# Optimization experiments

Hardware: AMD Instinct MI355X
Metric: run time of the kernel (lower is better)

The kernel has to match this reference:

```python
import jax, jax.numpy as jnp
import numpy as np
import math

V, T, E, N = 32000, 128, 64, 1024
SIGMA_MIN, SIGMA_MAX, C = 0.1, 10.0, 2.0


def setup_inputs() -> dict:
    key = jax.random.key(0)
    k1, k2, k3, k4, k5 = jax.random.split(key, 5)
    return {
        "x": jax.random.normal(k1, (T, N), dtype=jnp.float32),
        "mu": jax.random.normal(k2, (V, E), dtype=jnp.float32),
        "log_sigma": jax.random.normal(k3, (V, E), dtype=jnp.float32),
        "mu_c": jax.random.normal(k4, (T, E), dtype=jnp.float32),
        "log_sigma_c": jax.random.normal(k5, (T, E), dtype=jnp.float32),
        "t": 0,
    }


def reference(x, mu, log_sigma, mu_c, log_sigma_c, t):
    # parameter clamping done in-place in the torch forward
    bound = math.sqrt(C)
    mu = jnp.clip(mu, -bound, bound)
    mu_c = jnp.clip(mu_c, -bound, bound)
    log_sigma = jnp.clip(log_sigma, math.log(SIGMA_MIN), math.log(SIGMA_MAX))
    log_sigma_c = jnp.clip(log_sigma_c, math.log(SIGMA_MIN), math.log(SIGMA_MAX))

    sigma = jnp.exp(log_sigma)        # [V, E]
    sigma_c = jnp.exp(log_sigma_c)    # [T, E]

    # pairwise Gaussian expected-likelihood energy, vectorized over topics
    s = sigma[:, None, :] + sigma_c[None, :, :]            # [V, T, E]
    det_fac = jnp.sum(jnp.log(s), axis=-1)                 # [V, T]
    diff = mu[:, None, :] - mu_c[None, :, :]               # [V, T, E]
    diff_mu = jnp.sum(diff * diff / s, axis=-1)            # [V, T]
    emb_dim = mu.shape[-1]
    log_el = -0.5 * (det_fac + diff_mu + emb_dim * math.log(2.0 * math.pi))

    # per-topic softmax over the vocab axis
    w = jax.nn.softmax(log_el, axis=0)                     # [V, T]

    return w @ x.reshape(-1, x.shape[-1])                  # [V, N]
```

## Files before the change

### kernel.cpp

```cpp
#include <hip/hip_runtime.h>
#include <math.h>

#define VV 32000
#define TT 128
#define EE 64
#define NN 1024
#define NPART 500

static constexpr float BOUND    = 1.41421356237309515f;
static constexpr float LOG_SMIN = -2.30258509299404568f;
static constexpr float LOG_SMAX =  2.30258509299404568f;
static constexpr float LN2      =  0.69314718055994531f;
static constexpr float E_LOG2PI =  64.0f * 1.83787706640934548f;

typedef __attribute__((ext_vector_type(2)))  float f32x2;
typedef __attribute__((ext_vector_type(8)))  short short8;
typedef __attribute__((ext_vector_type(16))) float float16;

static __device__ inline unsigned short f2bf(float f) {
    union { float f; unsigned u; } v; v.f = f;
    unsigned r = v.u + 0x7FFFu + ((v.u >> 16) & 1u);
    return (unsigned short)(r >> 16);
}

__global__ __launch_bounds__(256) void prep_ctx(const float* __restrict__ mu_c,
                                                const float* __restrict__ log_sigma_c,
                                                float* __restrict__ sc,
                                                float* __restrict__ mc) {
    int i = blockIdx.x * 256 + threadIdx.x;
    if (i < TT * EE) {
        float ls = log_sigma_c[i];
        ls = fminf(fmaxf(ls, LOG_SMIN), LOG_SMAX);
        sc[i] = __expf(ls);
        float m = mu_c[i];
        mc[i] = fminf(fmaxf(m, -BOUND), BOUND);
    }
}

__global__ __launch_bounds__(256) void logits_kernel(const float* __restrict__ mu,
                                                     const float* __restrict__ log_sigma,
                                                     const float* __restrict__ sc,
                                                     const float* __restrict__ mc,
                                                     float* __restrict__ logitsT,
                                                     float* __restrict__ pm,
                                                     float* __restrict__ pl) {
    __shared__ float part[8][4][64];
    const int tid  = threadIdx.x;
    const int lane = tid & 63;
    const int wv   = tid >> 6;
    const int v0   = blockIdx.x * 64;
    const int t0   = blockIdx.y * 64;
    const int e0   = wv * 16;
    const int e0u  = __builtin_amdgcn_readfirstlane(wv) * 16;

    f32x2 sv[8], mv[8];
    {
        const float* __restrict__ lsp = log_sigma + (size_t)(v0 + lane) * EE + e0;
        const float* __restrict__ mup = mu        + (size_t)(v0 + lane) * EE + e0;
#pragma unroll
        for (int j = 0; j < 8; j++) {
            float a = lsp[2 * j], b = lsp[2 * j + 1];
            a = fminf(fmaxf(a, LOG_SMIN), LOG_SMAX);
            b = fminf(fmaxf(b, LOG_SMIN), LOG_SMAX);
            sv[j] = f32x2{__expf(a), __expf(b)};
            float c = mup[2 * j], d = mup[2 * j + 1];
            mv[j] = f32x2{fminf(fmaxf(c, -BOUND), BOUND), fminf(fmaxf(d, -BOUND), BOUND)};
        }
    }

    for (int tb = 0; tb < 8; tb++) {
        f32x2 q[8], p[8];
#pragma unroll
        for (int i = 0; i < 8; i++) { q[i] = f32x2{0.f, 0.f}; p[i] = f32x2{1.f, 1.f}; }
#pragma unroll
        for (int i = 0; i < 8; i++) {
            const int t = t0 + tb * 8 + i;
            const f32x2* __restrict__ srow = (const f32x2*)(sc + t * EE + e0u);
            const f32x2* __restrict__ mrow = (const f32x2*)(mc + t * EE + e0u);
#pragma unroll
            for (int j = 0; j < 8; j++) {
                f32x2 s = sv[j] + srow[j];
                p[i] *= s;
                f32x2 d = mv[j] - mrow[j];
                f32x2 r;
                r.x = __builtin_amdgcn_rcpf(s.x);
                r.y = __builtin_amdgcn_rcpf(s.y);
                q[i] += d * d * r;
            }
        }
#pragma unroll
        for (int i = 0; i < 8; i++) {
            float contrib = __log2f(p[i].x * p[i].y) * LN2 + q[i].x + q[i].y;
            part[i][wv][lane] = contrib;
        }
        __syncthreads();
#pragma unroll
        for (int k = 0; k < 2; k++) {
            const int i = wv * 2 + k;
            const int t = t0 + tb * 8 + i;
            float sum = part[i][0][lane] + part[i][1][lane] + part[i][2][lane] + part[i][3][lane];
            float logit = -0.5f * (sum + E_LOG2PI);
            logitsT[t * VV + v0 + lane] = logit;

            float m = logit;
#pragma unroll
            for (int off = 1; off < 64; off <<= 1) m = fmaxf(m, __shfl_xor(m, off));
            float sx = __expf(logit - m);
#pragma unroll
            for (int off = 1; off < 64; off <<= 1) sx += __shfl_xor(sx, off);
            if (lane == 0) {
                pm[t * NPART + blockIdx.x] = m;
                pl[t * NPART + blockIdx.x] = sx;
            }
        }
        __syncthreads();
    }
}

__global__ __launch_bounds__(256) void merge_xpose(const float* __restrict__ pm,
                                                   const float* __restrict__ pl,
                                                   const float* __restrict__ x,
                                                   float* __restrict__ stats,
                                                   unsigned short* __restrict__ xT) {
    const int tid = threadIdx.x;
    __shared__ float red[8];
    if (blockIdx.x < TT) {
        const int t = blockIdx.x;
        float m = -3.4e38f;
        for (int j = tid; j < NPART; j += 256) m = fmaxf(m, pm[t * NPART + j]);
#pragma unroll
        for (int off = 1; off < 64; off <<= 1) m = fmaxf(m, __shfl_xor(m, off));
        if ((tid & 63) == 0) red[tid >> 6] = m;
        __syncthreads();
        m = fmaxf(fmaxf(red[0], red[1]), fmaxf(red[2], red[3]));

        float l = 0.0f;
        for (int j = tid; j < NPART; j += 256)
            l += pl[t * NPART + j] * __expf(pm[t * NPART + j] - m);
#pragma unroll
        for (int off = 1; off < 64; off <<= 1) l += __shfl_xor(l, off);
        if ((tid & 63) == 0) red[4 + (tid >> 6)] = l;
        __syncthreads();
        if (tid == 0) {
            float tot = red[4] + red[5] + red[6] + red[7];
            stats[t] = m;
            stats[TT + t] = 1.0f / tot;
        }
    } else {
        const int b = blockIdx.x - TT;
        const int n = b * 128 + (tid & 127);
        const int th = tid >> 7;
        const float* __restrict__ xp = x + n;
#pragma unroll
        for (int i = 0; i < 64; i += 2) {
            int t = th * 64 + i;
            float x0 = xp[(size_t)t * NN];
            float x1 = xp[(size_t)(t + 1) * NN];
            *(unsigned*)&xT[n * TT + t] = (unsigned)f2bf(x0) | ((unsigned)f2bf(x1) << 16);
        }
    }
}

__global__ __launch_bounds__(256) void make_w(const float* __restrict__ logitsT,
                                              const float* __restrict__ stats,
                                              unsigned short* __restrict__ w) {
    __shared__ __attribute__((aligned(16))) unsigned short wl[64][136];
    __shared__ float sl[256];
    const int tid = threadIdx.x;
    const int v0 = blockIdx.x * 64;

    sl[tid] = stats[tid];
    __syncthreads();

    {
        const int v = tid & 63;
        const int tg = tid >> 6;
        const float* __restrict__ lp = logitsT + v0 + v;
#pragma unroll
        for (int i = 0; i < 32; i += 2) {
            int t = tg * 32 + i;
            float lg0 = lp[(size_t)t * VV];
            float lg1 = lp[(size_t)(t + 1) * VV];
            float w0 = __expf(lg0 - sl[t])     * sl[TT + t];
            float w1 = __expf(lg1 - sl[t + 1]) * sl[TT + t + 1];
            *(unsigned*)&wl[v][t] = (unsigned)f2bf(w0) | ((unsigned)f2bf(w1) << 16);
        }
    }
    __syncthreads();

    {
        const int v = tid >> 2;
        const int seg = (tid & 3) * 32;
#pragma unroll
        for (int j = 0; j < 4; j++) {
            uint4 d = *(const uint4*)&wl[v][seg + j * 8];
            *(uint4*)&w[(size_t)(v0 + v) * TT + seg + j * 8] = d;
        }
    }
}

__global__ __launch_bounds__(256) void wx_mfma(const unsigned short* __restrict__ w,
                                               const unsigned short* __restrict__ xT,
                                               float* __restrict__ out) {
    const int tid = threadIdx.x;
    const int v0 = blockIdx.x * 64;
    const int n0 = blockIdx.y * 128;
    const int lane = tid & 63;
    const int wv   = tid >> 6;
    const int vh   = (wv & 1) * 32;
    const int nh   = (wv >> 1) * 64;
    const int r32  = lane & 31;
    const int koff = (lane >> 5) * 8;

    const unsigned short* __restrict__ ap  = w  + (size_t)(v0 + vh + r32) * TT + koff;
    const unsigned short* __restrict__ bp0 = xT + (size_t)(n0 + nh + r32) * TT + koff;
    const unsigned short* __restrict__ bp1 = bp0 + 32 * TT;

    float16 acc0 = {0,0,0,0,0,0,0,0,0,0,0,0,0,0,0,0};
    float16 acc1 = {0,0,0,0,0,0,0,0,0,0,0,0,0,0,0,0};
#pragma unroll
    for (int kb = 0; kb < 8; kb++) {
        short8 a  = *(const short8*)(ap  + kb * 16);
        short8 b0 = *(const short8*)(bp0 + kb * 16);
        short8 b1 = *(const short8*)(bp1 + kb * 16);
        acc0 = __builtin_amdgcn_mfma_f32_32x32x16_bf16(a, b0, acc0, 0, 0, 0);
        acc1 = __builtin_amdgcn_mfma_f32_32x32x16_bf16(a, b1, acc1, 0, 0, 0);
    }

    const int col = lane & 31;
    const int rbase = 4 * (lane >> 5);
#pragma unroll
    for (int r = 0; r < 16; r++) {
        int row = (r & 3) + 8 * (r >> 2) + rbase;
        float* dst = out + (size_t)(v0 + vh + row) * NN + n0 + nh + col;
        dst[0]  = acc0[r];
        dst[32] = acc1[r];
    }
}

extern "C" void kernel_launch(void* const* d_in, const int* in_sizes, int n_in,
                              void* d_out, int out_size, void* d_ws, size_t ws_size,
                              hipStream_t stream) {
    const float* x           = (const float*)d_in[0];
    const float* mu          = (const float*)d_in[1];
    const float* log_sigma   = (const float*)d_in[2];
    const float* mu_c        = (const float*)d_in[3];
    const float* log_sigma_c = (const float*)d_in[4];
    float* out = (float*)d_out;

    float* ws      = (float*)d_ws;
    float* logitsT = ws;
    float* pm      = logitsT + (size_t)TT * VV;
    float* pl      = pm + (size_t)TT * NPART;
    float* stats   = pl + (size_t)TT * NPART;
    float* sc      = stats + 2 * TT;
    float* mc      = sc + TT * EE;
    unsigned short* w_bf16 = (unsigned short*)(mc + TT * EE);
    unsigned short* xT     = w_bf16 + (size_t)VV * TT;

    prep_ctx<<<(TT * EE + 255) / 256, 256, 0, stream>>>(mu_c, log_sigma_c, sc, mc);
    logits_kernel<<<dim3(VV / 64, 2), 256, 0, stream>>>(mu, log_sigma, sc, mc,
                                                        logitsT, pm, pl);
    merge_xpose<<<TT + NN / 128, 256, 0, stream>>>(pm, pl, x, stats, xT);
    make_w<<<VV / 64, 256, 0, stream>>>(logitsT, stats, w_bf16);
    wx_mfma<<<dim3(VV / 64, NN / 128), 256, 0, stream>>>(w_bf16, xT, out);
}
```

Measured before the change: 250.9 us.

## Split logits grid over more topic blocks, prefetch context rows, swap GEMM grid order

Moves the x transpose into the prep kernel, so merge_stats only reduces the softmax statistics. The logits kernel now uses 4 topic blocks of 32 instead of 2 of 64, which doubles the grid. It also loads the context sigma and mu rows into registers ahead of use with a double-buffered prefetch, replacing per-topic global loads. The wx GEMM grid is reordered so consecutive blocks share a w tile across n blocks. The cost is recomputing the clamp and exp of the vocab parameters for twice as many blocks, plus more synchronisation rounds per block.

```diff
diff --git a/kernel.cpp b/kernel.cpp
--- a/kernel.cpp
+++ b/kernel.cpp
@@ -23,17 +23,34 @@
     return (unsigned short)(r >> 16);
 }
 
-__global__ __launch_bounds__(256) void prep_ctx(const float* __restrict__ mu_c,
-                                                const float* __restrict__ log_sigma_c,
-                                                float* __restrict__ sc,
-                                                float* __restrict__ mc) {
-    int i = blockIdx.x * 256 + threadIdx.x;
-    if (i < TT * EE) {
-        float ls = log_sigma_c[i];
-        ls = fminf(fmaxf(ls, LOG_SMIN), LOG_SMAX);
-        sc[i] = __expf(ls);
-        float m = mu_c[i];
-        mc[i] = fminf(fmaxf(m, -BOUND), BOUND);
+__global__ __launch_bounds__(256) void prep_xpose(const float* __restrict__ mu_c,
+                                                  const float* __restrict__ log_sigma_c,
+                                                  const float* __restrict__ x,
+                                                  float* __restrict__ sc,
+                                                  float* __restrict__ mc,
+                                                  unsigned short* __restrict__ xT) {
+    const int tid = threadIdx.x;
+    if (blockIdx.x < 32) {
+        int i = blockIdx.x * 256 + tid;
+        if (i < TT * EE) {
+            float ls = log_sigma_c[i];
+            ls = fminf(fmaxf(ls, LOG_SMIN), LOG_SMAX);
+            sc[i] = __expf(ls);
+            float m = mu_c[i];
+            mc[i] = fminf(fmaxf(m, -BOUND), BOUND);
+        }
+    } else {
+        const int b = blockIdx.x - 32;
+        const int n = b * 128 + (tid & 127);
+        const int th = tid >> 7;
+        const float* __restrict__ xp = x + n;
+#pragma unroll
+        for (int i = 0; i < 64; i += 2) {
+            int t = th * 64 + i;
+            float x0 = xp[(size_t)t * NN];
+            float x1 = xp[(size_t)(t + 1) * NN];
+            *(unsigned*)&xT[n * TT + t] = (unsigned)f2bf(x0) | ((unsigned)f2bf(x1) << 16);
+        }
     }
 }
 
@@ -44,19 +61,18 @@
                                                      float* __restrict__ logitsT,
                                                      float* __restrict__ pm,
                                                      float* __restrict__ pl) {
-    __shared__ float part[8][4][64];
+    __shared__ float part[16][4][64];
     const int tid  = threadIdx.x;
     const int lane = tid & 63;
     const int wv   = tid >> 6;
     const int v0   = blockIdx.x * 64;
-    const int t0   = blockIdx.y * 64;
-    const int e0   = wv * 16;
+    const int t0   = blockIdx.y * 32;
     const int e0u  = __builtin_amdgcn_readfirstlane(wv) * 16;
 
     f32x2 sv[8], mv[8];
     {
-        const float* __restrict__ lsp = log_sigma + (size_t)(v0 + lane) * EE + e0;
-        const float* __restrict__ mup = mu        + (size_t)(v0 + lane) * EE + e0;
+        const float* __restrict__ lsp = log_sigma + (size_t)(v0 + lane) * EE + e0u;
+        const float* __restrict__ mup = mu        + (size_t)(v0 + lane) * EE + e0u;
 #pragma unroll
         for (int j = 0; j < 8; j++) {
             float a = lsp[2 * j], b = lsp[2 * j + 1];
@@ -68,36 +84,45 @@
         }
     }
 
-    for (int tb = 0; tb < 8; tb++) {
-        f32x2 q[8], p[8];
-#pragma unroll
-        for (int i = 0; i < 8; i++) { q[i] = f32x2{0.f, 0.f}; p[i] = f32x2{1.f, 1.f}; }
-#pragma unroll
-        for (int i = 0; i < 8; i++) {
-            const int t = t0 + tb * 8 + i;
-            const f32x2* __restrict__ srow = (const f32x2*)(sc + t * EE + e0u);
-            const f32x2* __restrict__ mrow = (const f32x2*)(mc + t * EE + e0u);
+    f32x2 cs[2][8], cm[2][8];
+    {
+        const f32x2* __restrict__ sp = (const f32x2*)(sc + t0 * EE + e0u);
+        const f32x2* __restrict__ mp = (const f32x2*)(mc + t0 * EE + e0u);
+#pragma unroll
+        for (int j = 0; j < 8; j++) { cs[0][j] = sp[j]; cm[0][j] = mp[j]; }
+    }
+
+    for (int tb = 0; tb < 2; tb++) {
+#pragma unroll
+        for (int i = 0; i < 16; i++) {
+            const int ti  = tb * 16 + i;
+            const int cur = ti & 1;
+            if (ti < 31) {
+                const int tn = t0 + ti + 1;
+                const f32x2* __restrict__ sp = (const f32x2*)(sc + tn * EE + e0u);
+                const f32x2* __restrict__ mp = (const f32x2*)(mc + tn * EE + e0u);
+#pragma unroll
+                for (int j = 0; j < 8; j++) { cs[cur ^ 1][j] = sp[j]; cm[cur ^ 1][j] = mp[j]; }
+            }
+            f32x2 q = {0.f, 0.f};
+            f32x2 p = {1.f, 1.f};
 #pragma unroll
             for (int j = 0; j < 8; j++) {
-                f32x2 s = sv[j] + srow[j];
-                p[i] *= s;
-                f32x2 d = mv[j] - mrow[j];
+                f32x2 s = sv[j] + cs[cur][j];
+                p *= s;
+                f32x2 d = mv[j] - cm[cur][j];
                 f32x2 r;
                 r.x = __builtin_amdgcn_rcpf(s.x);
                 r.y = __builtin_amdgcn_rcpf(s.y);
-                q[i] += d * d * r;
+                q += d * d * r;
             }
-        }
-#pragma unroll
-        for (int i = 0; i < 8; i++) {
-            float contrib = __log2f(p[i].x * p[i].y) * LN2 + q[i].x + q[i].y;
-            part[i][wv][lane] = contrib;
+            part[i][wv][lane] = __log2f(p.x * p.y) * LN2 + q.x + q.y;
         }
         __syncthreads();
 #pragma unroll
-        for (int k = 0; k < 2; k++) {
-            const int i = wv * 2 + k;
-            const int t = t0 + tb * 8 + i;
+        for (int k = 0; k < 4; k++) {
+            const int i = wv * 4 + k;
+            const int t = t0 + tb * 16 + i;
             float sum = part[i][0][lane] + part[i][1][lane] + part[i][2][lane] + part[i][3][lane];
             float logit = -0.5f * (sum + E_LOG2PI);
             logitsT[t * VV + v0 + lane] = logit;
@@ -117,47 +142,31 @@
     }
 }
 
-__global__ __launch_bounds__(256) void merge_xpose(const float* __restrict__ pm,
+__global__ __launch_bounds__(256) void merge_stats(const float* __restrict__ pm,
                                                    const float* __restrict__ pl,
-                                                   const float* __restrict__ x,
-                                                   float* __restrict__ stats,
-                                                   unsigned short* __restrict__ xT) {
-    const int tid = threadIdx.x;
+                                                   float* __restrict__ stats) {
+    const int tid = threadIdx.x;
+    const int t = blockIdx.x;
     __shared__ float red[8];
-    if (blockIdx.x < TT) {
-        const int t = blockIdx.x;
-        float m = -3.4e38f;
-        for (int j = tid; j < NPART; j += 256) m = fmaxf(m, pm[t * NPART + j]);
-#pragma unroll
-        for (int off = 1; off < 64; off <<= 1) m = fmaxf(m, __shfl_xor(m, off));
-        if ((tid & 63) == 0) red[tid >> 6] = m;
-        __syncthreads();
-        m = fmaxf(fmaxf(red[0], red[1]), fmaxf(red[2], red[3]));
-
-        float l = 0.0f;
-        for (int j = tid; j < NPART; j += 256)
-            l += pl[t * NPART + j] * __expf(pm[t * NPART + j] - m);
-#pragma unroll
-        for (int off = 1; off < 64; off <<= 1) l += __shfl_xor(l, off);
-        if ((tid & 63) == 0) red[4 + (tid >> 6)] = l;
-        __syncthreads();
-        if (tid == 0) {
-            float tot = red[4] + red[5] + red[6] + red[7];
-            stats[t] = m;
-            stats[TT + t] = 1.0f / tot;
-        }
-    } else {
-        const int b = blockIdx.x - TT;
-        const int n = b * 128 + (tid & 127);
-        const int th = tid >> 7;
-        const float* __restrict__ xp = x + n;
-#pragma unroll
-        for (int i = 0; i < 64; i += 2) {
-            int t = th * 64 + i;
-            float x0 = xp[(size_t)t * NN];
-            float x1 = xp[(size_t)(t + 1) * NN];
-            *(unsigned*)&xT[n * TT + t] = (unsigned)f2bf(x0) | ((unsigned)f2bf(x1) << 16);
-        }
+    float m = -3.4e38f;
+    for (int j = tid; j < NPART; j += 256) m = fmaxf(m, pm[t * NPART + j]);
+#pragma unroll
+    for (int off = 1; off < 64; off <<= 1) m = fmaxf(m, __shfl_xor(m, off));
+    if ((tid & 63) == 0) red[tid >> 6] = m;
+    __syncthreads();
+    m = fmaxf(fmaxf(red[0], red[1]), fmaxf(red[2], red[3]));
+
+    float l = 0.0f;
+    for (int j = tid; j < NPART; j += 256)
+        l += pl[t * NPART + j] * __expf(pm[t * NPART + j] - m);
+#pragma unroll
+    for (int off = 1; off < 64; off <<= 1) l += __shfl_xor(l, off);
+    if ((tid & 63) == 0) red[4 + (tid >> 6)] = l;
+    __syncthreads();
+    if (tid == 0) {
+        float tot = red[4] + red[5] + red[6] + red[7];
+        stats[t] = m;
+        stats[TT + t] = 1.0f / tot;
     }
 }
 
@@ -203,8 +212,8 @@
                                                const unsigned short* __restrict__ xT,
                                                float* __restrict__ out) {
     const int tid = threadIdx.x;
-    const int v0 = blockIdx.x * 64;
-    const int n0 = blockIdx.y * 128;
+    const int n0 = blockIdx.x * 128;
+    const int v0 = blockIdx.y * 64;
     const int lane = tid & 63;
     const int wv   = tid >> 6;
     const int vh   = (wv & 1) * 32;
@@ -258,10 +267,10 @@
     unsigned short* w_bf16 = (unsigned short*)(mc + TT * EE);
     unsigned short* xT     = w_bf16 + (size_t)VV * TT;
 
-    prep_ctx<<<(TT * EE + 255) / 256, 256, 0, stream>>>(mu_c, log_sigma_c, sc, mc);
-    logits_kernel<<<dim3(VV / 64, 2), 256, 0, stream>>>(mu, log_sigma, sc, mc,
+    prep_xpose<<<40, 256, 0, stream>>>(mu_c, log_sigma_c, x, sc, mc, xT);
+    logits_kernel<<<dim3(VV / 64, 4), 256, 0, stream>>>(mu, log_sigma, sc, mc,
                                                         logitsT, pm, pl);
-    merge_xpose<<<TT + NN / 128, 256, 0, stream>>>(pm, pl, x, stats, xT);
+    merge_stats<<<TT, 256, 0, stream>>>(pm, pl, stats);
     make_w<<<VV / 64, 256, 0, stream>>>(logitsT, stats, w_bf16);
-    wx_mfma<<<dim3(VV / 64, NN / 128), 256, 0, stream>>>(w_bf16, xT, out);
-}
+    wx_mfma<<<dim3(NN / 128, VV / 64), 256, 0, stream>>>(w_bf16, xT, out);
+}
```

Measured after the change: 246.7 us. About the same (-1.7%).
